# Performance work log

Hardware: AMD Instinct MI355X
Metric: run time of the kernel (lower is better)

The kernel has to match this reference:

```python
import jax, jax.numpy as jnp
import numpy as np

T, B, D_IN, H, OUT, CLIP = 512, 64, 256, 512, 128, 100.0


def lstm_dir(x, Wih, Whh, b, clip):
    # x: (T,B,D); Wih: (4H,D); Whh: (4H,H); b: (4H,) = b_ih + b_hh combined
    Bsz = x.shape[1]
    Hh = Whh.shape[1]
    xW = jnp.einsum('tbd,gd->tbg', x, Wih) + b  # (T,B,4H) precomputed input projection

    def step(carry, xw_t):
        h, c = carry
        gates = xw_t + h @ Whh.T
        i, f, g, o = jnp.split(gates, 4, axis=-1)  # torch gate order i,f,g,o
        i = jax.nn.sigmoid(i); f = jax.nn.sigmoid(f)
        g = jnp.tanh(g); o = jax.nn.sigmoid(o)
        c = jnp.clip(f * c + i * g, -clip, clip)   # cell-state clipping
        h = o * jnp.tanh(c)
        return (h, c), h

    h0 = jnp.zeros((Bsz, Hh), x.dtype)
    _, hs = jax.lax.scan(step, (h0, h0), xW)
    return hs  # (T,B,H)


def bilstm_layer(x, Wih, Whh, b, clip):
    # Wih: (2,4H,D) stacked [fwd, bwd]
    fwd = lstm_dir(x, Wih[0], Whh[0], b[0], clip)
    bwd = lstm_dir(x[::-1], Wih[1], Whh[1], b[1], clip)[::-1]
    return jnp.concatenate([fwd, bwd], axis=-1)  # (T,B,2H)


def setup_inputs() -> dict:
    key = jax.random.key(0)
    ks = jax.random.split(key, 12)
    s = 1.0 / np.sqrt(H)
    inp = {
        'input': jax.random.normal(ks[0], (T, B, D_IN), jnp.float32),
        'Wih0': jax.random.uniform(ks[1], (2, 4 * H, D_IN), jnp.float32, -s, s),
        'Whh0': jax.random.uniform(ks[2], (2, 4 * H, H), jnp.float32, -s, s),
        'b0': jax.random.uniform(ks[3], (2, 4 * H), jnp.float32, -s, s),
        'Wih1': jax.random.uniform(ks[4], (2, 4 * H, 2 * H), jnp.float32, -s, s),
        'Whh1': jax.random.uniform(ks[5], (2, 4 * H, H), jnp.float32, -s, s),
        'b1': jax.random.uniform(ks[6], (2, 4 * H), jnp.float32, -s, s),
        'Wa': jax.random.uniform(ks[7], (1, H), jnp.float32, -s, s),
        'ba': jax.random.uniform(ks[8], (1,), jnp.float32, -s, s),
        'Wo': jax.random.uniform(ks[9], (OUT, H), jnp.float32, -s, s),
        'bo': jax.random.uniform(ks[10], (OUT,), jnp.float32, -s, s),
    }
    return inp


def reference(input, Wih0, Whh0, b0, Wih1, Whh1, b1, Wa, ba, Wo, bo):
    h = bilstm_layer(input, Wih0, Whh0, b0, CLIP)   # (T,B,2H)
    h = bilstm_layer(h, Wih1, Whh1, b1, CLIP)       # (T,B,2H)
    t, b, _ = h.shape
    Hh = Whh0.shape[-1]
    h = h.reshape(t, b, 2, Hh)
    out = h[:, :, 0, :] + h[:, :, 1, :]             # fwd + bwd, (T,B,H)
    out = out.transpose(1, 0, 2)                    # (B,T,H)
    attn = out @ Wa.T + ba                          # (B,T,1)
    attn = jax.nn.softmax(attn, axis=1)
    pooled = jnp.sum(out * attn, axis=1)            # (B,H)
    pred = pooled @ Wo.T + bo                       # (B,OUT)
    return pred, attn
```

## Files before the change

kernel.cpp:

```cpp
#include <hip/hip_runtime.h>
#include <cstdint>
#include <cstddef>

#define TT 512
#define NWG 256
#define SCH0 32
#define NCH0 16
#define SCH1 16
#define NCH1 32

#define OFF_H0   0ul
#define SZ_H0    (512ul*1024ul*64ul*2ul)
#define OFF_OUT  (OFF_H0 + SZ_H0)
#define SZ_OUT   (512ul*512ul*64ul*4ul)
#define OFF_XW1  (OFF_OUT + SZ_OUT)
#define SZ_XW1   (2ul*32ul*2048ul*64ul*4ul)
#define OFF_HBUF (OFF_XW1 + SZ_XW1)
#define SZ_HBUF  (2ul*2ul*2ul*512ul*64ul*4ul)
#define OFF_CST  (OFF_HBUF + SZ_HBUF)
#define SZ_CST   (2ul*2ul*512ul*64ul*4ul)
#define OFF_FLG  (OFF_CST + SZ_CST)
#define SZ_FLG   (2ul*2ul*512ul*128ul*4ul)
#define OFF_E    (OFF_FLG + SZ_FLG)
#define SZ_E     (64ul*512ul*4ul)
#define OFF_AT   (OFF_E + SZ_E)
#define SZ_AT    (512ul*64ul*4ul)
#define OFF_POOL (OFF_AT + SZ_AT)
#define SZ_POOL  (512ul*64ul*4ul)

#define SZB0 (2ul*(size_t)SCH0*2048ul*64ul*4ul)
#define SZB1 (2ul*(size_t)SCH1*2048ul*64ul*4ul)

#define FUSED_LDS 53248

typedef unsigned long long u64;
typedef __attribute__((ext_vector_type(8))) short short8v;
typedef __attribute__((ext_vector_type(4))) float f32x4;

#define AHL(p) __hip_atomic_load((p), __ATOMIC_RELAXED, __HIP_MEMORY_SCOPE_AGENT)

__device__ __forceinline__ unsigned short f2bf(float f) {
  unsigned u = __float_as_uint(f);
  u += 0x7fffu + ((u >> 16) & 1u);
  return (unsigned short)(u >> 16);
}

__device__ __forceinline__ void gemm_tile_mfma(const float* __restrict__ X32,
                                               const unsigned short* __restrict__ Xb,
                                               const float* __restrict__ W,
                                               const float* __restrict__ bias,
                                               float* __restrict__ xwout,
                                               int s0, int sch, int gtile, int sl, int d,
                                               unsigned short* aWb, unsigned short* aWr,
                                               unsigned short* aXb, unsigned short* aXr) {
  const int K = X32 ? 256 : 1024;
  const int tid = threadIdx.x;
  const int sg = s0 + sl;
  const int t = d ? (511 - sg) : sg;
  const int w = tid >> 6, lane = tid & 63;
  const int lhi = lane >> 4, lcol = lane & 15;
  const int g0 = gtile*128;
  const float* Wbase = W + ((size_t)d*2048 + g0)*K;

  f32x4 acc[8];
  #pragma unroll
  for (int mt = 0; mt < 8; ++mt) acc[mt] = (f32x4){0.f,0.f,0.f,0.f};

  for (int kc = 0; kc < K; kc += 64) {
    __syncthreads();
    #pragma unroll
    for (int i = 0; i < 4; ++i) {
      const int p = i*256 + tid;
      const int row = p >> 3, o = p & 7;
      const float* src = Wbase + (size_t)row*K + kc + o*8;
      const float4 v0 = *(const float4*)(src);
      const float4 v1 = *(const float4*)(src + 4);
      const float f[8] = {v0.x,v0.y,v0.z,v0.w,v1.x,v1.y,v1.z,v1.w};
      short8v vb, vr;
      #pragma unroll
      for (int e = 0; e < 8; ++e) {
        const unsigned short hb = f2bf(f[e]);
        vb[e] = (short)hb;
        vr[e] = (short)f2bf(f[e] - __uint_as_float((unsigned)hb << 16));
      }
      const int os = o ^ (row & 7);
      *(short8v*)(aWb + (size_t)row*64 + os*8) = vb;
      *(short8v*)(aWr + (size_t)row*64 + os*8) = vr;
    }
    if (X32) {
      #pragma unroll
      for (int i = 0; i < 4; ++i) {
        const int p = i*256 + tid;
        const int bb = p >> 4, kq = p & 15;
        const float4 v = *(const float4*)(X32 + ((size_t)t*64 + bb)*256 + kc + kq*4);
        const float f[4] = {v.x, v.y, v.z, v.w};
        #pragma unroll
        for (int j = 0; j < 4; ++j) {
          const int k = kq*4 + j;
          const int o = k >> 3, e = k & 7;
          const unsigned short hb = f2bf(f[j]);
          const unsigned short hr = f2bf(f[j] - __uint_as_float((unsigned)hb << 16));
          aXb[((o*64 + bb)<<3) + e] = hb;
          aXr[((o*64 + bb)<<3) + e] = hr;
        }
      }
    } else {
      const unsigned short* Xbase = Xb + (size_t)t*K*64;
      #pragma unroll
      for (int i = 0; i < 4; ++i) {
        const int p = i*256 + tid;
        const int k = p >> 4, b4 = (p & 15) << 2;
        const uint2 r = *(const uint2*)(Xbase + (size_t)(kc + k)*64 + b4);
        const int o = k >> 3, e = k & 7;
        aXb[((o*64 + b4+0)<<3) + e] = (unsigned short)(r.x & 0xffffu);
        aXb[((o*64 + b4+1)<<3) + e] = (unsigned short)(r.x >> 16);
        aXb[((o*64 + b4+2)<<3) + e] = (unsigned short)(r.y & 0xffffu);
        aXb[((o*64 + b4+3)<<3) + e] = (unsigned short)(r.y >> 16);
      }
    }
    __syncthreads();
    #pragma unroll
    for (int ks = 0; ks < 2; ++ks) {
      const int xoff = (((ks*4 + lhi)*64) + w*16 + lcol)*8;
      const short8v xb = *(const short8v*)(aXb + xoff);
      #pragma unroll
      for (int mt = 0; mt < 8; ++mt) {
        const int row = mt*16 + lcol;
        const int os = (ks*4 + lhi) ^ (row & 7);
        const short8v ab = *(const short8v*)(aWb + (size_t)row*64 + os*8);
        const short8v ar = *(const short8v*)(aWr + (size_t)row*64 + os*8);
        acc[mt] = __builtin_amdgcn_mfma_f32_16x16x32_bf16(ab, xb, acc[mt], 0, 0, 0);
        if (X32) {
          const short8v xr = *(const short8v*)(aXr + xoff);
          acc[mt] = __builtin_amdgcn_mfma_f32_16x16x32_bf16(ab, xr, acc[mt], 0, 0, 0);
        }
        acc[mt] = __builtin_amdgcn_mfma_f32_16x16x32_bf16(ar, xb, acc[mt], 0, 0, 0);
      }
    }
  }
  float* op = xwout + (((size_t)d*sch + sl)*2048 + g0)*64 + w*16 + lcol;
  const float* bp = bias + d*2048 + g0;
  #pragma unroll
  for (int mt = 0; mt < 8; ++mt) {
    #pragma unroll
    for (int r = 0; r < 4; ++r) {
      const int grow = mt*16 + lhi*4 + r;
      op[(size_t)grow*64] = acc[mt][r] + bp[grow];
    }
  }
}

__device__ __forceinline__ void gemm_tile(const float* __restrict__ X32,
                                          const unsigned short* __restrict__ Xb,
                                          const float* __restrict__ W,
                                          const float* __restrict__ bias,
                                          float* __restrict__ xwout,
                                          int s0, int sch, int gtile, int sl, int d,
                                          float* lds) {
  unsigned short* aWb = (unsigned short*)lds;
  unsigned short* aWr = aWb + 8192;
  unsigned short* aXb = aWr + 8192;
  unsigned short* aXr = aXb + 4096;
  gemm_tile_mfma(X32, Xb, W, bias, xwout, s0, sch, gtile, sl, d, aWb, aWr, aXb, aXr);
}

__global__ void __launch_bounds__(256) xw_gemm(const float* __restrict__ X32,
                                               const unsigned short* __restrict__ Xb,
                                               const float* __restrict__ W,
                                               const float* __restrict__ bias,
                                               float* __restrict__ xwout,
                                               int s0, int sch) {
  __shared__ float lds_s[12288];
  gemm_tile(X32, Xb, W, bias, xwout, s0, sch, blockIdx.x, blockIdx.y, blockIdx.z, lds_s);
}

__device__ __forceinline__ void recur_body(
    const float* __restrict__ Whh, const float* __restrict__ xw,
    char* __restrict__ wsb, int layer, int s0, int sch, float* lds)
{
  unsigned short* alds = (unsigned short*)lds;

  unsigned short* h0 = (unsigned short*)(wsb + OFF_H0);
  float* outsum  = (float*)(wsb + OFF_OUT);
  unsigned* hbase = (unsigned*)(wsb + OFF_HBUF) + (size_t)layer*131072;
  float* cstore  = (float*)(wsb + OFF_CST);
  unsigned* flg  = (unsigned*)(wsb + OFF_FLG);

  const int tid = threadIdx.x;
  const int d     = blockIdx.x >> 7;
  const int slot  = blockIdx.x & 127;
  const int jbase = slot << 2;

  const int w    = tid >> 6;
  const int lane = tid & 63;
  const int lhi  = lane >> 4;
  const int lcol = lane & 15;
  const int jj   = lhi;
  const int b    = w*16 + lcol;

  __builtin_amdgcn_s_setprio(1);

  for (int m = 0; m < 16; ++m) {
    const int g = m & 3, j = m >> 2;
    const float* src = Whh + ((size_t)d*2048 + g*512 + jbase + j)*512;
    for (int k = tid; k < 512; k += 256) {
      const float wv = src[k];
      const unsigned short wb = f2bf(wv);
      const unsigned short wr = f2bf(wv - __uint_as_float((unsigned)wb << 16));
      const int oct = (k >> 3) & 3;
      const int idx = (((k >> 5)*4 + oct)*16 + (m ^ oct))*8 + (k & 7);
      alds[idx] = wb;
      alds[8192 + idx] = wr;
    }
  }
  float creg = cstore[((size_t)(layer*2 + d)*512 + jbase + jj)*64 + b];
  __syncthreads();

  const unsigned fbase = (unsigned)(layer*2 + d) * 512u;

  for (int sl = 0; sl < sch; ++sl) {
    const int sg = s0 + sl;
    const int t_in = d ? (511 - sg) : sg;

    const float* xwp = xw + ((size_t)(d*sch + sl)*2048 + (size_t)(jbase + jj))*64 + b;
    const float px0 = xwp[0];
    const float px1 = xwp[32768];
    const float px2 = xwp[65536];
    const float px3 = xwp[98304];

    if (sg > 0) {
      if (tid < 128) {
        unsigned* p = &flg[(size_t)(fbase + (unsigned)sg - 1u)*128 + tid];
        while (AHL(p) == 0u) __builtin_amdgcn_s_sleep(1);
      }
      __syncthreads();
    }

    const u64* hsrc = (const u64*)(hbase + ((sg & 1)*2 + d)*32768);

    u64 ring[8][4];
    #pragma unroll
    for (int ks = 0; ks < 8; ++ks) {
      const size_t hb0 = (size_t)((ks*4 + lhi)*4)*64 + b;
      ring[ks][0] = AHL(hsrc + hb0);
      ring[ks][1] = AHL(hsrc + hb0 + 64);
      ring[ks][2] = AHL(hsrc + hb0 + 128);
      ring[ks][3] = AHL(hsrc + hb0 + 192);
    }

    f32x4 acc = {0.f, 0.f, 0.f, 0.f};
    #pragma unroll
    for (int ks = 0; ks < 16; ++ks) {
      const u64 q0 = ring[ks & 7][0], q1 = ring[ks & 7][1];
      const u64 q2 = ring[ks & 7][2], q3 = ring[ks & 7][3];
      if (ks < 8) {
        const size_t hb2 = (size_t)(((ks + 8)*4 + lhi)*4)*64 + b;
        ring[ks][0] = AHL(hsrc + hb2);
        ring[ks][1] = AHL(hsrc + hb2 + 64);
        ring[ks][2] = AHL(hsrc + hb2 + 128);
        ring[ks][3] = AHL(hsrc + hb2 + 192);
      }
      union { unsigned u[4]; short8v v; } hb, rb;
      hb.u[0] = __builtin_amdgcn_perm((unsigned)(q0 >> 32), (unsigned)q0, 0x07060302u);
      rb.u[0] = __builtin_amdgcn_perm((unsigned)(q0 >> 32), (unsigned)q0, 0x05040100u);
      hb.u[1] = __builtin_amdgcn_perm((unsigned)(q1 >> 32), (unsigned)q1, 0x07060302u);
      rb.u[1] = __builtin_amdgcn_perm((unsigned)(q1 >> 32), (unsigned)q1, 0x05040100u);
      hb.u[2] = __builtin_amdgcn_perm((unsigned)(q2 >> 32), (unsigned)q2, 0x07060302u);
      rb.u[2] = __builtin_amdgcn_perm((unsigned)(q2 >> 32), (unsigned)q2, 0x05040100u);
      hb.u[3] = __builtin_amdgcn_perm((unsigned)(q3 >> 32), (unsigned)q3, 0x07060302u);
      rb.u[3] = __builtin_amdgcn_perm((unsigned)(q3 >> 32), (unsigned)q3, 0x05040100u);
      const int abase = ((ks*4 + lhi)*16 + (lcol ^ lhi))*8;
      const short8v ab = *(const short8v*)(alds + abase);
      const short8v ar = *(const short8v*)(alds + 8192 + abase);
      acc = __builtin_amdgcn_mfma_f32_16x16x32_bf16(ab, hb.v, acc, 0, 0, 0);
      acc = __builtin_amdgcn_mfma_f32_16x16x32_bf16(ab, rb.v, acc, 0, 0, 0);
      acc = __builtin_amdgcn_mfma_f32_16x16x32_bf16(ar, hb.v, acc, 0, 0, 0);
    }

    const float pi = acc[0] + px0;
    const float pf = acc[1] + px1;
    const float pg = acc[2] + px2;
    const float po = acc[3] + px3;
    const float iv = 1.0f/(1.0f + __expf(-pi));
    const float fv = 1.0f/(1.0f + __expf(-pf));
    const float gv = tanhf(pg);
    const float ov = 1.0f/(1.0f + __expf(-po));
    float cc2 = fv*creg + iv*gv;
    cc2 = fminf(fmaxf(cc2, -100.0f), 100.0f);
    creg = cc2;
    const float h = ov*tanhf(cc2);

    const unsigned short hb16 = f2bf(h);
    const unsigned short rb16 = f2bf(h - __uint_as_float((unsigned)hb16 << 16));
    const unsigned hpk = ((unsigned)hb16 << 16) | (unsigned)rb16;
    unsigned* hout = hbase + (((sg & 1) ^ 1)*2 + d)*32768;
    const int kj = jbase + jj;
    __hip_atomic_store(hout + ((size_t)(kj >> 1)*128 + b*2 + (kj & 1)), hpk,
                       __ATOMIC_RELAXED, __HIP_MEMORY_SCOPE_AGENT);

    __syncthreads();
    if (tid == 0)
      __hip_atomic_store(&flg[(size_t)(fbase + (unsigned)sg)*128 + slot], 1u,
                         __ATOMIC_RELAXED, __HIP_MEMORY_SCOPE_AGENT);
    if (layer == 0) {
      h0[(size_t)t_in*65536 + (size_t)(d*512 + kj)*64 + b] = hb16;
    } else {
      atomicAdd(&outsum[(size_t)t_in*32768 + (size_t)kj*64 + b], h);
    }
  }
  cstore[((size_t)(layer*2 + d)*512 + jbase + jj)*64 + b] = creg;
}

__global__ void __launch_bounds__(256, 2) fused_step(
    const float* __restrict__ Whh, const float* __restrict__ xw_cur,
    float* __restrict__ xw_next,
    const float* __restrict__ gX32, const unsigned short* __restrict__ gXb,
    const float* __restrict__ gW, const float* __restrict__ gB,
    char* __restrict__ wsb,
    int rlayer, int rs0, int rsch,
    int gs0, int gsch, int gnjobs)
{
  extern __shared__ float lds[];
  if (blockIdx.x < NWG) {
    recur_body(Whh, xw_cur, wsb, rlayer, rs0, rsch, lds);
  } else {
    const int wg = blockIdx.x - NWG;
    const int half = gnjobs >> 1;
    for (int job = wg; job < gnjobs; job += NWG) {
      const int dd  = (job >= half) ? 1 : 0;
      const int rem = job - (dd ? half : 0);
      const int sl  = rem >> 4;
      const int gt  = rem & 15;
      gemm_tile(gX32, gXb, gW, gB, xw_next, gs0, gsch, gt, sl, dd, lds);
    }
  }
}

__global__ void __launch_bounds__(256) attn_logits(const float* __restrict__ outsum,
                                                   const float* __restrict__ Wa,
                                                   const float* __restrict__ ba,
                                                   float* __restrict__ e) {
  __shared__ float part[4*64];
  const int t = blockIdx.x;
  const int b = threadIdx.x & 63, jq = threadIdx.x >> 6;
  const float* base = outsum + (size_t)t * 512 * 64;
  float acc = 0.0f;
  for (int j = jq*128; j < jq*128 + 128; ++j)
    acc += base[j*64 + b] * Wa[j];
  part[jq*64 + b] = acc;
  __syncthreads();
  if (threadIdx.x < 64) {
    const int bb = threadIdx.x;
    e[bb*512 + t] = part[0*64+bb] + part[1*64+bb] + part[2*64+bb] + part[3*64+bb] + ba[0];
  }
}

__global__ void __launch_bounds__(256) attn_softmax(const float* __restrict__ e,
                                                    float* __restrict__ attn,
                                                    float* __restrict__ aT) {
  __shared__ float red[256];
  const int b = blockIdx.x, tid = threadIdx.x;
  const float v0 = e[b*512 + tid];
  const float v1 = e[b*512 + 256 + tid];
  red[tid] = fmaxf(v0, v1);
  __syncthreads();
  for (int st = 128; st; st >>= 1) { if (tid < st) red[tid] = fmaxf(red[tid], red[tid+st]); __syncthreads(); }
  const float M = red[0];
  __syncthreads();
  const float e0 = __expf(v0 - M), e1 = __expf(v1 - M);
  red[tid] = e0 + e1;
  __syncthreads();
  for (int st = 128; st; st >>= 1) { if (tid < st) red[tid] += red[tid+st]; __syncthreads(); }
  const float inv = 1.0f / red[0];
  const float a0 = e0*inv, a1 = e1*inv;
  attn[b*512 + tid]       = a0;
  attn[b*512 + 256 + tid] = a1;
  aT[tid*64 + b]       = a0;
  aT[(256+tid)*64 + b] = a1;
}

__global__ void __launch_bounds__(256) attn_pool(const float* __restrict__ outsum,
                                                 const float* __restrict__ aT,
                                                 float* __restrict__ pooled) {
  const int tid = threadIdx.x;
  const int b = tid & 63, jj = tid >> 6;
  const int j = blockIdx.x*4 + jj;
  float acc = 0.0f;
  #pragma unroll 4
  for (int t = 0; t < 512; ++t)
    acc += aT[t*64 + b] * outsum[((size_t)t*512 + j)*64 + b];
  pooled[j*64 + b] = acc;
}

__global__ void __launch_bounds__(128) pred_kern(const float* __restrict__ pooled,
                                                 const float* __restrict__ Wo,
                                                 const float* __restrict__ bo,
                                                 float* __restrict__ out) {
  const int b = blockIdx.x, o = threadIdx.x;
  float acc = bo[o];
  const float* wr = Wo + o*512;
  #pragma unroll 4
  for (int j = 0; j < 512; j += 4) {
    const float4 w = *(const float4*)(wr + j);
    acc += w.x*pooled[(j+0)*64 + b] + w.y*pooled[(j+1)*64 + b]
         + w.z*pooled[(j+2)*64 + b] + w.w*pooled[(j+3)*64 + b];
  }
  out[b*128 + o] = acc;
}

extern "C" void kernel_launch(void* const* d_in, const int* in_sizes, int n_in,
                              void* d_out, int out_size, void* d_ws, size_t ws_size,
                              hipStream_t stream) {
  (void)in_sizes; (void)n_in; (void)out_size; (void)ws_size;
  const float* x    = (const float*)d_in[0];
  const float* Wih0 = (const float*)d_in[1];
  const float* Whh0 = (const float*)d_in[2];
  const float* b0   = (const float*)d_in[3];
  const float* Wih1 = (const float*)d_in[4];
  const float* Whh1 = (const float*)d_in[5];
  const float* b1   = (const float*)d_in[6];
  const float* Wa   = (const float*)d_in[7];
  const float* ba   = (const float*)d_in[8];
  const float* Wo   = (const float*)d_in[9];
  const float* bo   = (const float*)d_in[10];
  float* out = (float*)d_out;
  char* wsb  = (char*)d_ws;

  hipMemsetAsync(wsb + OFF_HBUF, 0, SZ_HBUF + SZ_CST + SZ_FLG, stream);

  float* xw0[2] = { (float*)(wsb + OFF_OUT), (float*)(wsb + OFF_OUT + SZB0) };
  float* xw1[2] = { (float*)(wsb + OFF_XW1), (float*)(wsb + OFF_XW1 + SZB1) };
  const unsigned short* h0p = (const unsigned short*)(wsb + OFF_H0);

  xw_gemm<<<dim3(16, SCH0, 2), 256, 0, stream>>>(x, nullptr, Wih0, b0, xw0[0], 0, SCH0);

  for (int c = 0; c < NCH0; ++c) {
    const bool last = (c == NCH0 - 1);
    fused_step<<<dim3(2*NWG), dim3(256), FUSED_LDS, stream>>>(
        Whh0, xw0[c & 1], xw0[(c + 1) & 1],
        x, nullptr, Wih0, b0,
        wsb, 0, c*SCH0, SCH0,
        (c + 1)*SCH0, SCH0, last ? 0 : 16*SCH0*2);
  }

  xw_gemm<<<dim3(16, SCH1, 2), 256, 0, stream>>>(nullptr, h0p, Wih1, b1, xw1[0], 0, SCH1);

  hipMemsetAsync(wsb + OFF_OUT, 0, SZ_OUT, stream);

  for (int c = 0; c < NCH1; ++c) {
    const bool last = (c == NCH1 - 1);
    fused_step<<<dim3(2*NWG), dim3(256), FUSED_LDS, stream>>>(
        Whh1, xw1[c & 1], xw1[(c + 1) & 1],
        nullptr, h0p, Wih1, b1,
        wsb, 1, c*SCH1, SCH1,
        (c + 1)*SCH1, SCH1, last ? 0 : 16*SCH1*2);
  }

  attn_logits <<<512, 256, 0, stream>>>((float*)(wsb + OFF_OUT), Wa, ba, (float*)(wsb + OFF_E));
  attn_softmax<<< 64, 256, 0, stream>>>((float*)(wsb + OFF_E), out + 8192, (float*)(wsb + OFF_AT));
  attn_pool   <<<128, 256, 0, stream>>>((float*)(wsb + OFF_OUT), (float*)(wsb + OFF_AT),
                                        (float*)(wsb + OFF_POOL));
  pred_kern   <<< 64, 128, 0, stream>>>((float*)(wsb + OFF_POOL), Wo, bo, out);
}
```

Measured before the change: 7.301 ms.

## Split recurrent workgroups by batch half and K-split with LDS reduction

Each recurrent workgroup now owns 8 hidden units for half the batch (32 columns) instead of 4 units for the full batch. Each wave splits the K dimension in half and computes two row blocks, and partial sums are exchanged through a new LDS reduction area. Flag waits now cover only the 64 workgroups of the same batch half. This halves the h-vector loads per wave and shortens the dependent MFMA chain per step, at the cost of larger LDS use (which may reduce occupancy), an extra barrier per step, and twice the weight rows per workgroup.

```diff
diff --git a/kernel.cpp b/kernel.cpp
--- a/kernel.cpp
+++ b/kernel.cpp
@@ -31,7 +31,7 @@
 #define SZB0 (2ul*(size_t)SCH0*2048ul*64ul*4ul)
 #define SZB1 (2ul*(size_t)SCH1*2048ul*64ul*4ul)
 
-#define FUSED_LDS 53248
+#define FUSED_LDS 69632
 
 typedef unsigned long long u64;
 typedef __attribute__((ext_vector_type(8))) short short8v;
@@ -179,6 +179,7 @@
     char* __restrict__ wsb, int layer, int s0, int sch, float* lds)
 {
   unsigned short* alds = (unsigned short*)lds;
+  float4* red4 = (float4*)(lds + 16384);
 
   unsigned short* h0 = (unsigned short*)(wsb + OFF_H0);
   float* outsum  = (float*)(wsb + OFF_OUT);
@@ -186,51 +187,59 @@
   float* cstore  = (float*)(wsb + OFF_CST);
   unsigned* flg  = (unsigned*)(wsb + OFF_FLG);
 
-  const int tid = threadIdx.x;
-  const int d     = blockIdx.x >> 7;
-  const int slot  = blockIdx.x & 127;
-  const int jbase = slot << 2;
+  const int tid  = threadIdx.x;
+  const int d    = blockIdx.x >> 7;
+  const int bg   = (blockIdx.x >> 6) & 1;
+  const int slot = blockIdx.x & 63;
 
   const int w    = tid >> 6;
   const int lane = tid & 63;
+  const int kh   = w >> 1;
+  const int cw   = w & 1;
   const int lhi  = lane >> 4;
   const int lcol = lane & 15;
-  const int jj   = lhi;
-  const int b    = w*16 + lcol;
+  const int jown = slot*8 + kh*4 + lhi;
+  const int bidx = bg*32 + cw*16 + lcol;
 
   __builtin_amdgcn_s_setprio(1);
 
-  for (int m = 0; m < 16; ++m) {
-    const int g = m & 3, j = m >> 2;
-    const float* src = Whh + ((size_t)d*2048 + g*512 + jbase + j)*512;
-    for (int k = tid; k < 512; k += 256) {
-      const float wv = src[k];
-      const unsigned short wb = f2bf(wv);
-      const unsigned short wr = f2bf(wv - __uint_as_float((unsigned)wb << 16));
-      const int oct = (k >> 3) & 3;
-      const int idx = (((k >> 5)*4 + oct)*16 + (m ^ oct))*8 + (k & 7);
-      alds[idx] = wb;
-      alds[8192 + idx] = wr;
-    }
-  }
-  float creg = cstore[((size_t)(layer*2 + d)*512 + jbase + jj)*64 + b];
+  for (int rw = 0; rw < 2; ++rw) {
+    for (int r16 = 0; r16 < 16; ++r16) {
+      const int g = r16 & 3, jj = r16 >> 2;
+      const float* src = Whh + ((size_t)d*2048 + g*512 + slot*8 + rw*4 + jj)*512;
+      for (int k = tid; k < 512; k += 256) {
+        const float wv = src[k];
+        const unsigned short wb = f2bf(wv);
+        const unsigned short wr = f2bf(wv - __uint_as_float((unsigned)wb << 16));
+        const int khs = k >> 8, kl = k & 255;
+        const int ks2 = kl >> 5, oct = (kl >> 3) & 3, e = kl & 7;
+        const int idx = ((ks2*4 + oct)*16 + (r16 ^ oct))*8 + e;
+        unsigned short* blk = alds + (size_t)((rw*2 + khs)*2)*4096;
+        blk[idx] = wb;
+        blk[4096 + idx] = wr;
+      }
+    }
+  }
+  float creg = cstore[((size_t)(layer*2 + d)*512 + jown)*64 + bidx];
   __syncthreads();
 
   const unsigned fbase = (unsigned)(layer*2 + d) * 512u;
+  const unsigned short* a0b = alds + (size_t)(kh*2)*4096;
+  const unsigned short* a1b = alds + (size_t)((4 + kh*2))*4096;
 
   for (int sl = 0; sl < sch; ++sl) {
     const int sg = s0 + sl;
     const int t_in = d ? (511 - sg) : sg;
 
-    const float* xwp = xw + ((size_t)(d*sch + sl)*2048 + (size_t)(jbase + jj))*64 + b;
+    const float* xwp = xw + ((size_t)(d*sch + sl)*2048 + (size_t)jown)*64 + bidx;
     const float px0 = xwp[0];
     const float px1 = xwp[32768];
     const float px2 = xwp[65536];
     const float px3 = xwp[98304];
 
     if (sg > 0) {
-      if (tid < 128) {
-        unsigned* p = &flg[(size_t)(fbase + (unsigned)sg - 1u)*128 + tid];
+      if (tid < 64) {
+        unsigned* p = &flg[(size_t)(fbase + (unsigned)sg - 1u)*128 + bg*64 + tid];
         while (AHL(p) == 0u) __builtin_amdgcn_s_sleep(1);
       }
       __syncthreads();
@@ -238,23 +247,26 @@
 
     const u64* hsrc = (const u64*)(hbase + ((sg & 1)*2 + d)*32768);
 
-    u64 ring[8][4];
+    u64 ring[4][4];
     #pragma unroll
-    for (int ks = 0; ks < 8; ++ks) {
-      const size_t hb0 = (size_t)((ks*4 + lhi)*4)*64 + b;
+    for (int ks = 0; ks < 4; ++ks) {
+      const int g8 = kh*32 + ks*4 + lhi;
+      const size_t hb0 = (size_t)(g8*4)*64 + bidx;
       ring[ks][0] = AHL(hsrc + hb0);
       ring[ks][1] = AHL(hsrc + hb0 + 64);
       ring[ks][2] = AHL(hsrc + hb0 + 128);
       ring[ks][3] = AHL(hsrc + hb0 + 192);
     }
 
-    f32x4 acc = {0.f, 0.f, 0.f, 0.f};
+    f32x4 acc0 = {0.f,0.f,0.f,0.f};
+    f32x4 acc1 = {0.f,0.f,0.f,0.f};
     #pragma unroll
-    for (int ks = 0; ks < 16; ++ks) {
-      const u64 q0 = ring[ks & 7][0], q1 = ring[ks & 7][1];
-      const u64 q2 = ring[ks & 7][2], q3 = ring[ks & 7][3];
-      if (ks < 8) {
-        const size_t hb2 = (size_t)(((ks + 8)*4 + lhi)*4)*64 + b;
+    for (int ks = 0; ks < 8; ++ks) {
+      const u64 q0 = ring[ks & 3][0], q1 = ring[ks & 3][1];
+      const u64 q2 = ring[ks & 3][2], q3 = ring[ks & 3][3];
+      if (ks < 4) {
+        const int g8 = kh*32 + (ks + 4)*4 + lhi;
+        const size_t hb2 = (size_t)(g8*4)*64 + bidx;
         ring[ks][0] = AHL(hsrc + hb2);
         ring[ks][1] = AHL(hsrc + hb2 + 64);
         ring[ks][2] = AHL(hsrc + hb2 + 128);
@@ -269,18 +281,32 @@
       rb.u[2] = __builtin_amdgcn_perm((unsigned)(q2 >> 32), (unsigned)q2, 0x05040100u);
       hb.u[3] = __builtin_amdgcn_perm((unsigned)(q3 >> 32), (unsigned)q3, 0x07060302u);
       rb.u[3] = __builtin_amdgcn_perm((unsigned)(q3 >> 32), (unsigned)q3, 0x05040100u);
-      const int abase = ((ks*4 + lhi)*16 + (lcol ^ lhi))*8;
-      const short8v ab = *(const short8v*)(alds + abase);
-      const short8v ar = *(const short8v*)(alds + 8192 + abase);
-      acc = __builtin_amdgcn_mfma_f32_16x16x32_bf16(ab, hb.v, acc, 0, 0, 0);
-      acc = __builtin_amdgcn_mfma_f32_16x16x32_bf16(ab, rb.v, acc, 0, 0, 0);
-      acc = __builtin_amdgcn_mfma_f32_16x16x32_bf16(ar, hb.v, acc, 0, 0, 0);
-    }
-
-    const float pi = acc[0] + px0;
-    const float pf = acc[1] + px1;
-    const float pg = acc[2] + px2;
-    const float po = acc[3] + px3;
+      const int inner = ((ks*4 + lhi)*16 + (lcol ^ lhi))*8;
+      const short8v ab0 = *(const short8v*)(a0b + inner);
+      const short8v ar0 = *(const short8v*)(a0b + 4096 + inner);
+      acc0 = __builtin_amdgcn_mfma_f32_16x16x32_bf16(ab0, hb.v, acc0, 0, 0, 0);
+      acc0 = __builtin_amdgcn_mfma_f32_16x16x32_bf16(ab0, rb.v, acc0, 0, 0, 0);
+      acc0 = __builtin_amdgcn_mfma_f32_16x16x32_bf16(ar0, hb.v, acc0, 0, 0, 0);
+      const short8v ab1 = *(const short8v*)(a1b + inner);
+      const short8v ar1 = *(const short8v*)(a1b + 4096 + inner);
+      acc1 = __builtin_amdgcn_mfma_f32_16x16x32_bf16(ab1, hb.v, acc1, 0, 0, 0);
+      acc1 = __builtin_amdgcn_mfma_f32_16x16x32_bf16(ab1, rb.v, acc1, 0, 0, 0);
+      acc1 = __builtin_amdgcn_mfma_f32_16x16x32_bf16(ar1, hb.v, acc1, 0, 0, 0);
+    }
+
+    if (kh == 0) red4[(size_t)(2 + cw)*64 + lane] = make_float4(acc1[0],acc1[1],acc1[2],acc1[3]);
+    else         red4[(size_t)(0 + cw)*64 + lane] = make_float4(acc0[0],acc0[1],acc0[2],acc0[3]);
+    __syncthreads();
+    f32x4 own = (kh == 0) ? acc0 : acc1;
+    {
+      const float4 p = red4[(size_t)(kh*2 + cw)*64 + lane];
+      own[0] += p.x; own[1] += p.y; own[2] += p.z; own[3] += p.w;
+    }
+
+    const float pi = own[0] + px0;
+    const float pf = own[1] + px1;
+    const float pg = own[2] + px2;
+    const float po = own[3] + px3;
     const float iv = 1.0f/(1.0f + __expf(-pi));
     const float fv = 1.0f/(1.0f + __expf(-pf));
     const float gv = tanhf(pg);
@@ -294,21 +320,20 @@
     const unsigned short rb16 = f2bf(h - __uint_as_float((unsigned)hb16 << 16));
     const unsigned hpk = ((unsigned)hb16 << 16) | (unsigned)rb16;
     unsigned* hout = hbase + (((sg & 1) ^ 1)*2 + d)*32768;
-    const int kj = jbase + jj;
-    __hip_atomic_store(hout + ((size_t)(kj >> 1)*128 + b*2 + (kj & 1)), hpk,
+    __hip_atomic_store(hout + ((size_t)(jown >> 1)*128 + bidx*2 + (jown & 1)), hpk,
                        __ATOMIC_RELAXED, __HIP_MEMORY_SCOPE_AGENT);
 
     __syncthreads();
     if (tid == 0)
-      __hip_atomic_store(&flg[(size_t)(fbase + (unsigned)sg)*128 + slot], 1u,
+      __hip_atomic_store(&flg[(size_t)(fbase + (unsigned)sg)*128 + bg*64 + slot], 1u,
                          __ATOMIC_RELAXED, __HIP_MEMORY_SCOPE_AGENT);
     if (layer == 0) {
-      h0[(size_t)t_in*65536 + (size_t)(d*512 + kj)*64 + b] = hb16;
+      h0[(size_t)t_in*65536 + (size_t)(d*512 + jown)*64 + bidx] = hb16;
     } else {
-      atomicAdd(&outsum[(size_t)t_in*32768 + (size_t)kj*64 + b], h);
-    }
-  }
-  cstore[((size_t)(layer*2 + d)*512 + jbase + jj)*64 + b] = creg;
+      atomicAdd(&outsum[(size_t)t_in*32768 + (size_t)jown*64 + bidx], h);
+    }
+  }
+  cstore[((size_t)(layer*2 + d)*512 + jown)*64 + bidx] = creg;
 }
 
 __global__ void __launch_bounds__(256, 2) fused_step(
```

Result: faster. 6.163 ms (-15.6%).
